# Optimization experiments

Measured on AMD Instinct MI355X. Metric: run time of the kernel, lower is better.

The kernel has to match this reference:

```python
import jax, jax.numpy as jnp
import numpy as np

N, LAT, H, R, L = 384, 64, 128, 16, 3
CUTOFF = 12.0
COORD_INIT_SCALE = 0.001


def setup_inputs() -> dict:
    key = jax.random.key(0)
    ks = jax.random.split(key, 12)
    def w(k, shape, fan):
        return jax.random.normal(k, shape, jnp.float32) / np.float32(np.sqrt(fan))
    return {
        "z": jax.random.normal(ks[0], (N, LAT), jnp.float32),
        # spread anchors so the radius graph is non-trivially sparse
        "anchor_coords": jax.random.normal(ks[1], (N, 3), jnp.float32) * 10.0,
        "proj_W": w(ks[2], (LAT, H), LAT),
        "proj_b": jnp.zeros((H,), jnp.float32),
        "eW1": w(ks[3], (L, 2 * H + R, H), 2 * H + R),
        "eb1": jnp.zeros((L, H), jnp.float32),
        "eW2": w(ks[4], (L, H, H), H),
        "eb2": jnp.zeros((L, H), jnp.float32),
        "nW1": w(ks[5], (L, 2 * H, H), 2 * H),
        "nb1": jnp.zeros((L, H), jnp.float32),
        "nW2": w(ks[6], (L, H, H), H),
        "nb2": jnp.zeros((L, H), jnp.float32),
        "cW1": w(ks[7], (L, H, H), H),
        "cb1": jnp.zeros((L, H), jnp.float32),
        # coord head scaled by coord_update_init_scale for stable coordinate updates
        "cW2": w(ks[8], (L, H, 1), H) * COORD_INIT_SCALE,
    }


def _rbf(d):
    # Gaussian radial basis expansion over [0, cutoff]
    mu = jnp.linspace(0.0, CUTOFF, R, dtype=d.dtype)            # (R,)
    gamma = jnp.asarray((R / CUTOFF) ** 2, d.dtype)
    return jnp.exp(-gamma * (d[..., None] - mu) ** 2)           # (..., R)


def reference(z, anchor_coords, proj_W, proj_b, eW1, eb1, eW2, eb2,
              nW1, nb1, nW2, nb2, cW1, cb1, cW2):
    silu = jax.nn.silu
    n = z.shape[0]
    h = z @ proj_W + proj_b                                      # (N, H)
    x = anchor_coords - anchor_coords.mean(0, keepdims=True)     # (N, 3)

    idx = jnp.arange(n)
    seq_mask = jnp.abs(idx[:, None] - idx[None, :]) == 1         # sequential edges
    eye = jnp.eye(n, dtype=bool)

    for l in range(L):
        # rebuild radius graph from current coords (dense jit-safe mask)
        diff = x[:, None, :] - x[None, :, :]                     # (N, N, 3) x_i - x_j
        d2 = jnp.sum(diff * diff, axis=-1)                       # (N, N)
        mask = ((d2 < CUTOFF ** 2) & ~eye) | seq_mask            # (N, N) bool
        maskf = mask.astype(h.dtype)
        d = jnp.sqrt(jnp.where(mask, d2, 1.0)) * maskf           # NaN-safe sqrt
        e = _rbf(d)                                              # (N, N, R)

        hi = jnp.broadcast_to(h[:, None, :], (n, n, H))          # receiver
        hj = jnp.broadcast_to(h[None, :, :], (n, n, H))          # sender
        m = silu(jnp.concatenate([hi, hj, e], -1) @ eW1[l] + eb1[l])
        m = silu(m @ eW2[l] + eb2[l]) * maskf[..., None]         # (N, N, H) messages

        agg = m.sum(1)                                           # scatter-add at receiver
        h = h + silu(jnp.concatenate([h, agg], -1) @ nW1[l] + nb1[l]) @ nW2[l] + nb2[l]

        w = (silu(m @ cW1[l] + cb1[l]) @ cW2[l]) * maskf[..., None]  # (N, N, 1)
        x = x + jnp.sum(diff * w, axis=1)                        # equivariant coord update
    return x
```

## Files before the change

kernel.cpp:

```cpp
#include <hip/hip_runtime.h>
#include <hip/hip_bf16.h>

#define NN 384
#define CUTOFF2 144.0f
#define GAMMA 1.7777778f

#define PK_L 26624
#define PK_WE 8192
#define PK_W2 10240
#define PK_C1 18432

#define STG_F32 1152
#define EDGE_SMEM ((PK_L + 8*STG_F32)*4)

#define O_XA 0
#define O_XB 4608
#define O_H 9216
#define O_A 205824
#define O_AGG 402432
#define O_HBF 599040
#define O_EREC 697344
#define O_UNITS 3056640
#define O_UCNT 3075072
#define O_PK 3075200

typedef __bf16 bf16x8 __attribute__((ext_vector_type(8)));
typedef float f32x4 __attribute__((ext_vector_type(4)));
typedef unsigned long long u64;

union ER { struct { float dx, dy, dz; unsigned j; } e; uint4 u4; };

__device__ __forceinline__ unsigned short f2bf(float f){
  unsigned u = __float_as_uint(f);
  return (unsigned short)((u + 0x7fffu + ((u >> 16) & 1u)) >> 16);
}
__device__ __forceinline__ unsigned pk2(float a, float b){
  return ((unsigned)f2bf(b) << 16) | f2bf(a);
}
__device__ __forceinline__ float silu(float x){ return x / (1.0f + __expf(-x)); }

__global__ void k_prep(const float* __restrict__ eW1, const float* __restrict__ eW2,
                       const float* __restrict__ cW1, unsigned* __restrict__ pk,
                       const float* __restrict__ anchor, float* __restrict__ xA,
                       float* __restrict__ xB, int* __restrict__ ucnt){
  if (blockIdx.x == 312) {
    __shared__ float ssum[3];
    int t = threadIdx.x;
    if (t < 3) { ssum[t] = 0.f; ucnt[t] = 0; }
    __syncthreads();
    for (int n = t; n < 384; n += 256) {
      atomicAdd(&ssum[0], anchor[n*3]);
      atomicAdd(&ssum[1], anchor[n*3+1]);
      atomicAdd(&ssum[2], anchor[n*3+2]);
    }
    __syncthreads();
    float m0 = ssum[0]*(1.f/384.f), m1 = ssum[1]*(1.f/384.f), m2 = ssum[2]*(1.f/384.f);
    for (int n = t; n < 384; n += 256) {
      float v0 = anchor[n*3]-m0, v1 = anchor[n*3+1]-m1, v2 = anchor[n*3+2]-m2;
      xA[n*3]=v0; xA[n*3+1]=v1; xA[n*3+2]=v2;
      xB[n*3]=v0; xB[n*3+1]=v1; xB[n*3+2]=v2;
    }
    return;
  }
  int t = blockIdx.x * 256 + threadIdx.x;
  int layer = t / PK_L, r = t % PK_L;
  const float* src; int fr; int isWe = 0;
  if (r < PK_WE)        { fr = r;          src = eW1 + (layer*272 + 128)*128; }
  else if (r < PK_W2)   { fr = r - PK_WE;  src = eW1 + (layer*272 + 256)*128; isWe = 1; }
  else if (r < PK_C1)   { fr = r - PK_W2;  src = eW2 + layer*128*128; }
  else                  { fr = r - PK_C1;  src = cW1 + layer*128*128; }
  int tp = fr & 3, l = (fr >> 2) & 63, nc = fr >> 8;
  int n, k;
  if (!isWe) { n = nc >> 2; int c = nc & 3; k = c*32 + ((l>>4)<<3) + 2*tp; }
  else       { n = nc;                      k = ((l>>4)<<3) + 2*tp; }
  int nn = n*16 + (l & 15);
  float w0, w1;
  if (isWe) { w0 = (k < 16)   ? src[k*128+nn]     : 0.f;
              w1 = (k+1 < 16) ? src[(k+1)*128+nn] : 0.f; }
  else      { w0 = src[k*128+nn]; w1 = src[(k+1)*128+nn]; }
  pk[t] = ((unsigned)f2bf(w1) << 16) | f2bf(w0);
}

__device__ __forceinline__ void scan_tail(
    int row, int rowsel, int t256, bool v, const float* __restrict__ x,
    uint4* __restrict__ erec, int* __restrict__ units, int* __restrict__ ucntSlot,
    int* scn){
  int* scnt  = scn + rowsel*2;
  int* sbase = scnt + 1;
  if (t256 == 0) *scnt = 0;
  __syncthreads();
  if (v) {
    float xi0 = x[row*3], xi1 = x[row*3+1], xi2 = x[row*3+2];
    for (int j = t256; j < 384; j += 256) {
      float d0 = xi0-x[j*3], d1 = xi1-x[j*3+1], d2 = xi2-x[j*3+2];
      float dd = d0*d0 + d1*d1 + d2*d2;
      bool msk = ((dd < CUTOFF2) && (j != row)) || (j == row-1) || (j == row+1);
      if (msk) {
        int ss = atomicAdd(scnt, 1);
        ER er; er.e.dx = d0; er.e.dy = d1; er.e.dz = d2; er.e.j = (unsigned)j;
        erec[row*384 + ss] = er.u4;
      }
    }
  }
  __syncthreads();
  if (v) {
    int cnt = *scnt;
    int p = (32 - (cnt & 31)) & 31;
    if (t256 < p) {
      ER er; er.e.dx = 0.f; er.e.dy = 0.f; er.e.dz = 0.f; er.e.j = (unsigned)row;
      erec[row*384 + cnt + t256] = er.u4;
    }
    if (t256 == 0) *sbase = atomicAdd(ucntSlot, (cnt + 31) >> 5);
  }
  __syncthreads();
  if (v) {
    int cnt = *scnt, nu = (cnt + 31) >> 5;
    if (t256 < nu) {
      int nv = cnt - (t256 << 5); if (nv > 32) nv = 32;
      units[*sbase + t256] = row | (t256 << 9) | (nv << 13);
    }
  }
}

__global__ __launch_bounds__(512) void k_projscan(
    const float* __restrict__ z, const float* __restrict__ pW,
    const float* __restrict__ pb, const float* __restrict__ eW1,
    const float* __restrict__ eb1, float* __restrict__ h,
    unsigned short* __restrict__ hbf, float* __restrict__ A,
    float* __restrict__ agg, const float* __restrict__ x,
    uint4* __restrict__ erec, int* __restrict__ units, int* __restrict__ ucntSlot){
  __shared__ float sb2[2*768];
  __shared__ int scn[4];
  const int tid = threadIdx.x;
  const int rowsel = tid >> 8, half = (tid >> 7) & 1, o = tid & 127, t256 = tid & 255;
  const int row = blockIdx.x + 256*rowsel;
  const bool v = row < NN;
  float* sb = sb2 + rowsel*768;
  float* sh = sb; float* part = sb + 512; float* sz = sb + 640;

  if (v) {
    if (half == 0) { if (o < 64) sz[o] = z[row*64 + o]; }
    else           agg[row*128 + o] = 0.f;
  }
  __syncthreads();
  float pp = 0.f;
  if (v) {
    int k0 = half*32;
    float p0=0,p1=0,p2=0,p3=0;
    #pragma unroll 8
    for (int k = k0; k < k0+32; k += 4) {
      p0 += sz[k]   * pW[k*128 + o];
      p1 += sz[k+1] * pW[(k+1)*128 + o];
      p2 += sz[k+2] * pW[(k+2)*128 + o];
      p3 += sz[k+3] * pW[(k+3)*128 + o];
    }
    pp = (p0+p1)+(p2+p3);
    if (half) part[o] = pp;
  }
  __syncthreads();
  if (v && !half) {
    float hh = pb[o] + pp + part[o];
    h[row*128 + o] = hh; sh[o] = hh;
    hbf[row*128 + o] = f2bf(hh);
  }
  __syncthreads();
  float cc = 0.f;
  if (v) {
    int k0 = half*64;
    float c0=0,c1=0,c2=0,c3=0;
    #pragma unroll 16
    for (int k = k0; k < k0+64; k += 4) {
      c0 += sh[k]   * eW1[k*128 + o];
      c1 += sh[k+1] * eW1[(k+1)*128 + o];
      c2 += sh[k+2] * eW1[(k+2)*128 + o];
      c3 += sh[k+3] * eW1[(k+3)*128 + o];
    }
    cc = (c0+c1)+(c2+c3);
    if (half) part[o] = cc;
  }
  __syncthreads();
  if (v && !half) A[row*128 + o] = eb1[o] + cc + part[o];

  scan_tail(row, rowsel, t256, v, x, erec, units, ucntSlot, scn);
}

__global__ __launch_bounds__(512) void k_node(
    const float* __restrict__ nW1, const float* __restrict__ nb1,
    const float* __restrict__ nW2, const float* __restrict__ nb2,
    const float* __restrict__ eW1n, const float* __restrict__ eb1n,
    float* __restrict__ h, unsigned short* __restrict__ hbf,
    float* __restrict__ agg, float* __restrict__ A,
    const float* __restrict__ xsrc, float* __restrict__ xdst,
    uint4* __restrict__ erec, int* __restrict__ units, int* __restrict__ ucntSlot){
  __shared__ float sb2[2*768];
  __shared__ int scn[4];
  const int tid = threadIdx.x;
  const int rowsel = tid >> 8, half = (tid >> 7) & 1, o = tid & 127, t256 = tid & 255;
  const int row = blockIdx.x + 256*rowsel;
  const bool v = row < NN;
  float* sb = sb2 + rowsel*768;
  float* sh = sb; float* sg = sb+128; float* st = sb+256; float* shn = sb+384; float* part = sb+512;

  if (v) {
    if (half == 0) {
      sh[o] = h[row*128 + o];
      if (o < 3) xdst[row*3 + o] = xsrc[row*3 + o];
    } else {
      sg[o] = agg[row*128 + o]; agg[row*128 + o] = 0.f;
    }
  }
  __syncthreads();
  float aa = 0.f;
  if (v) {
    const float* src = half ? sg : sh;
    const float* wb  = nW1 + half*128*128;
    float a0=0,a1=0,a2=0,a3=0;
    #pragma unroll 16
    for (int k = 0; k < 128; k += 4) {
      a0 += src[k]   * wb[k*128 + o];
      a1 += src[k+1] * wb[(k+1)*128 + o];
      a2 += src[k+2] * wb[(k+2)*128 + o];
      a3 += src[k+3] * wb[(k+3)*128 + o];
    }
    aa = (a0+a1)+(a2+a3);
    if (half) part[o] = aa;
  }
  __syncthreads();
  if (v && !half) st[o] = silu(nb1[o] + aa + part[o]);
  __syncthreads();
  float bb = 0.f;
  if (v) {
    int k0 = half*64;
    float b0=0,b1=0,b2=0,b3=0;
    #pragma unroll 16
    for (int k = k0; k < k0+64; k += 4) {
      b0 += st[k]   * nW2[k*128 + o];
      b1 += st[k+1] * nW2[(k+1)*128 + o];
      b2 += st[k+2] * nW2[(k+2)*128 + o];
      b3 += st[k+3] * nW2[(k+3)*128 + o];
    }
    bb = (b0+b1)+(b2+b3);
    if (half) part[o] = bb;
  }
  __syncthreads();
  if (v && !half) {
    float hn = sh[o] + nb2[o] + bb + part[o];
    h[row*128 + o] = hn; shn[o] = hn;
    hbf[row*128 + o] = f2bf(hn);
  }
  __syncthreads();
  float cc = 0.f;
  if (v) {
    int k0 = half*64;
    float c0=0,c1=0,c2=0,c3=0;
    #pragma unroll 16
    for (int k = k0; k < k0+64; k += 4) {
      c0 += shn[k]   * eW1n[k*128 + o];
      c1 += shn[k+1] * eW1n[(k+1)*128 + o];
      c2 += shn[k+2] * eW1n[(k+2)*128 + o];
      c3 += shn[k+3] * eW1n[(k+3)*128 + o];
    }
    cc = (c0+c1)+(c2+c3);
    if (half) part[o] = cc;
  }
  __syncthreads();
  if (v && !half) A[row*128 + o] = eb1n[o] + cc + part[o];

  scan_tail(row, rowsel, t256, v, xsrc, erec, units, ucntSlot, scn);
}

#define TRANSFORM(VA, VB, FA, FB)                                              \
  _Pragma("unroll")                                                            \
  for (int c = 0; c < 4; ++c) {                                                \
    _Pragma("unroll")                                                          \
    for (int tl = 0; tl < 2; ++tl) {                                           \
      int t = 2*c + tl;                                                        \
      _Pragma("unroll")                                                        \
      for (int r = 0; r < 4; ++r) {                                            \
        stg[(quad*4 + r)*36 + tl*16 + col0] = VA[t][r];                        \
        stg[(16 + quad*4 + r)*36 + tl*16 + col0] = VB[t][r];                   \
      }                                                                        \
    }                                                                          \
    float4 lo = *(const float4*)(stg + col0*36 + quad*8);                      \
    float4 hi = *(const float4*)(stg + col0*36 + quad*8 + 4);                  \
    FA[c].u = make_uint4(pk2(lo.x,lo.y), pk2(lo.z,lo.w),                       \
                         pk2(hi.x,hi.y), pk2(hi.z,hi.w));                      \
    float4 lo2 = *(const float4*)(stg + (16 + col0)*36 + quad*8);              \
    float4 hi2 = *(const float4*)(stg + (16 + col0)*36 + quad*8 + 4);          \
    FB[c].u = make_uint4(pk2(lo2.x,lo2.y), pk2(lo2.z,lo2.w),                   \
                         pk2(hi2.x,hi2.y), pk2(hi2.z,hi2.w));                  \
  }

__global__ __launch_bounds__(512, 1) void k_edge(
    float* __restrict__ x_out, const float* __restrict__ Ag,
    const unsigned short* __restrict__ hbf, const uint4* __restrict__ erec,
    const int* __restrict__ units, const int* __restrict__ Ucnt,
    float* __restrict__ agg, const unsigned* __restrict__ pkl,
    const float* __restrict__ eb2g, const float* __restrict__ cb1g,
    const float* __restrict__ cw2g){
  extern __shared__ unsigned smem[];
  const int tid = threadIdx.x, q = tid & 63, s = tid >> 6;
  const int U = Ucnt[0];
  if (blockIdx.x >= U) return;

  for (int idx = tid; idx < PK_L/4; idx += 512)
    ((uint4*)smem)[idx] = ((const uint4*)pkl)[idx];
  __syncthreads();

  const int col0 = q & 15, quad = q >> 4;
  float eb2v[8], cb1v[8], cw2v[8];
  #pragma unroll
  for (int t = 0; t < 8; ++t) {
    int c = t*16 + col0;
    eb2v[t] = eb2g[c]; cb1v[t] = cb1g[c]; cw2v[t] = cw2g[c];
  }
  float* stg = (float*)(smem + PK_L) + s*STG_F32;
  const f32x4 z4 = {0.f, 0.f, 0.f, 0.f};
  union U8 { uint4 u; bf16x8 v; };

  for (int u = blockIdx.x + 256*s; u < U; u += 2048) {
    const int desc = units[u];
    const int i = desc & 511, b = (desc >> 9) & 15, nvalid = (desc >> 13) & 63;
    float Aval[8];
    #pragma unroll
    for (int t = 0; t < 8; ++t) Aval[t] = Ag[i*128 + t*16 + col0];
    ER e0, e1;
    e0.u4 = erec[i*384 + b*32 + col0];
    e1.u4 = erec[i*384 + b*32 + 16 + col0];
    const int j0 = (int)e0.e.j, j1 = (int)e1.e.j;
    const float d0x = e0.e.dx, d0y = e0.e.dy, d0z = e0.e.dz;
    const float d1x = e1.e.dx, d1y = e1.e.dy, d1z = e1.e.dz;
    const float dd0 = sqrtf(d0x*d0x + d0y*d0y + d0z*d0z);
    const float dd1 = sqrtf(d1x*d1x + d1y*d1y + d1z*d1z);

    U8 ha0[4], ha1[4];
    #pragma unroll
    for (int c = 0; c < 4; ++c) {
      ha0[c].u = *(const uint4*)(hbf + j0*128 + c*32 + quad*8);
      ha1[c].u = *(const uint4*)(hbf + j1*128 + c*32 + quad*8);
    }

    U8 cve0, cve1;
    if (q < 32) {
      #pragma unroll
      for (int tp = 0; tp < 4; ++tp) {
        float k0 = (float)(quad*8 + 2*tp);
        float t00 = dd0 - 0.8f*k0, t01 = dd0 - 0.8f*(k0+1.f);
        float t10 = dd1 - 0.8f*k0, t11 = dd1 - 0.8f*(k0+1.f);
        (&cve0.u.x)[tp] = pk2(__expf(-GAMMA*t00*t00), __expf(-GAMMA*t01*t01));
        (&cve1.u.x)[tp] = pk2(__expf(-GAMMA*t10*t10), __expf(-GAMMA*t11*t11));
      }
    } else { cve0.u = make_uint4(0,0,0,0); cve1.u = make_uint4(0,0,0,0); }

    f32x4 acc0[8], acc1[8];
    #pragma unroll
    for (int t = 0; t < 8; ++t) { acc0[t] = z4; acc1[t] = z4; }
    #pragma unroll
    for (int t = 0; t < 8; ++t) {
      #pragma unroll
      for (int c = 0; c < 4; ++c) {
        bf16x8 w = *(const bf16x8*)(smem + ((t*4 + c)*64 + q)*4);
        acc0[t] = __builtin_amdgcn_mfma_f32_16x16x32_bf16(ha0[c].v, w, acc0[t], 0, 0, 0);
        acc1[t] = __builtin_amdgcn_mfma_f32_16x16x32_bf16(ha1[c].v, w, acc1[t], 0, 0, 0);
      }
      bf16x8 we = *(const bf16x8*)(smem + PK_WE + (t*64 + q)*4);
      acc0[t] = __builtin_amdgcn_mfma_f32_16x16x32_bf16(cve0.v, we, acc0[t], 0, 0, 0);
      acc1[t] = __builtin_amdgcn_mfma_f32_16x16x32_bf16(cve1.v, we, acc1[t], 0, 0, 0);
    }
    #pragma unroll
    for (int t = 0; t < 8; ++t)
      #pragma unroll
      for (int r = 0; r < 4; ++r) {
        acc0[t][r] = silu(acc0[t][r] + Aval[t]);
        acc1[t][r] = silu(acc1[t][r] + Aval[t]);
      }

    U8 a20[4], a21[4];
    TRANSFORM(acc0, acc1, a20, a21);

    f32x4 m0[8], m1v[8];
    #pragma unroll
    for (int t = 0; t < 8; ++t) { m0[t] = z4; m1v[t] = z4; }
    #pragma unroll
    for (int t = 0; t < 8; ++t)
      #pragma unroll
      for (int c = 0; c < 4; ++c) {
        bf16x8 w = *(const bf16x8*)(smem + PK_W2 + ((t*4 + c)*64 + q)*4);
        m0[t] = __builtin_amdgcn_mfma_f32_16x16x32_bf16(a20[c].v, w, m0[t], 0, 0, 0);
        m1v[t] = __builtin_amdgcn_mfma_f32_16x16x32_bf16(a21[c].v, w, m1v[t], 0, 0, 0);
      }
    #pragma unroll
    for (int t = 0; t < 8; ++t) {
      float cs = 0.f;
      #pragma unroll
      for (int r = 0; r < 4; ++r) {
        m0[t][r] = silu(m0[t][r] + eb2v[t]);
        m1v[t][r] = silu(m1v[t][r] + eb2v[t]);
        if (quad*4 + r < nvalid) cs += m0[t][r];
        if (16 + quad*4 + r < nvalid) cs += m1v[t][r];
      }
      cs += __shfl_xor(cs, 16); cs += __shfl_xor(cs, 32);
      if (q < 16) atomicAdd(&agg[i*128 + t*16 + q], cs);
    }

    U8 a30[4], a31[4];
    TRANSFORM(m0, m1v, a30, a31);

    f32x4 c30[8], c31[8];
    #pragma unroll
    for (int t = 0; t < 8; ++t) { c30[t] = z4; c31[t] = z4; }
    #pragma unroll
    for (int t = 0; t < 8; ++t)
      #pragma unroll
      for (int c = 0; c < 4; ++c) {
        bf16x8 w = *(const bf16x8*)(smem + PK_C1 + ((t*4 + c)*64 + q)*4);
        c30[t] = __builtin_amdgcn_mfma_f32_16x16x32_bf16(a30[c].v, w, c30[t], 0, 0, 0);
        c31[t] = __builtin_amdgcn_mfma_f32_16x16x32_bf16(a31[c].v, w, c31[t], 0, 0, 0);
      }
    float p0[4], p1[4];
    #pragma unroll
    for (int r = 0; r < 4; ++r) {
      float pa = 0.f, pb = 0.f;
      #pragma unroll
      for (int t = 0; t < 8; ++t) {
        pa += silu(c30[t][r] + cb1v[t]) * cw2v[t];
        pb += silu(c31[t][r] + cb1v[t]) * cw2v[t];
      }
      if (quad*4 + r >= nvalid) pa = 0.f;
      if (16 + quad*4 + r >= nvalid) pb = 0.f;
      p0[r] = pa; p1[r] = pb;
    }
    #pragma unroll
    for (int r = 0; r < 4; ++r)
      #pragma unroll
      for (int off = 1; off < 16; off <<= 1) {
        p0[r] += __shfl_xor(p0[r], off);
        p1[r] += __shfl_xor(p1[r], off);
      }
    float dx0 = 0.f, dx1 = 0.f, dx2 = 0.f;
    #pragma unroll
    for (int r = 0; r < 4; ++r) {
      int el = quad*4 + r;
      float s0 = __shfl(d0x, el), s1 = __shfl(d0y, el), s2 = __shfl(d0z, el);
      if (col0 == 0) { dx0 += p0[r]*s0; dx1 += p0[r]*s1; dx2 += p0[r]*s2; }
      float u0 = __shfl(d1x, el), u1 = __shfl(d1y, el), u2 = __shfl(d1z, el);
      if (col0 == 0) { dx0 += p1[r]*u0; dx1 += p1[r]*u1; dx2 += p1[r]*u2; }
    }
    dx0 += __shfl_xor(dx0, 16); dx0 += __shfl_xor(dx0, 32);
    dx1 += __shfl_xor(dx1, 16); dx1 += __shfl_xor(dx1, 32);
    dx2 += __shfl_xor(dx2, 16); dx2 += __shfl_xor(dx2, 32);
    if (q == 0) {
      atomicAdd(&x_out[i*3 + 0], dx0);
      atomicAdd(&x_out[i*3 + 1], dx1);
      atomicAdd(&x_out[i*3 + 2], dx2);
    }
  }
}

extern "C" void kernel_launch(void* const* d_in, const int* in_sizes, int n_in,
                              void* d_out, int out_size, void* d_ws, size_t ws_size,
                              hipStream_t stream){
  const float* z      = (const float*)d_in[0];
  const float* anchor = (const float*)d_in[1];
  const float* projW  = (const float*)d_in[2];
  const float* projb  = (const float*)d_in[3];
  const float* eW1    = (const float*)d_in[4];
  const float* eb1    = (const float*)d_in[5];
  const float* eW2    = (const float*)d_in[6];
  const float* eb2    = (const float*)d_in[7];
  const float* nW1    = (const float*)d_in[8];
  const float* nb1    = (const float*)d_in[9];
  const float* nW2    = (const float*)d_in[10];
  const float* nb2    = (const float*)d_in[11];
  const float* cW1    = (const float*)d_in[12];
  const float* cb1    = (const float*)d_in[13];
  const float* cW2    = (const float*)d_in[14];
  float* out = (float*)d_out;

  char* w = (char*)d_ws;
  float* xA  = (float*)(w + O_XA);
  float* xB  = (float*)(w + O_XB);
  float* h   = (float*)(w + O_H);
  float* A   = (float*)(w + O_A);
  float* agg = (float*)(w + O_AGG);
  unsigned short* hbf = (unsigned short*)(w + O_HBF);
  uint4* erec = (uint4*)(w + O_EREC);
  int* units = (int*)(w + O_UNITS);
  int* ucnt  = (int*)(w + O_UCNT);
  unsigned* pk = (unsigned*)(w + O_PK);

  hipFuncSetAttribute((const void*)k_edge, hipFuncAttributeMaxDynamicSharedMemorySize, EDGE_SMEM);

  k_prep<<<313, 256, 0, stream>>>(eW1, eW2, cW1, pk, anchor, xA, xB, ucnt);
  k_projscan<<<256, 512, 0, stream>>>(z, projW, projb, eW1, eb1, h, hbf, A, agg,
                                      xA, erec, units, ucnt + 0);
  k_edge<<<256, 512, EDGE_SMEM, stream>>>(xB, A, hbf, erec, units, ucnt + 0,
                                          agg, pk, eb2, cb1, cW2);
  k_node<<<256, 512, 0, stream>>>(nW1, nb1, nW2, nb2, eW1 + 272*128, eb1 + 128,
                                  h, hbf, agg, A, xB, xA, erec, units, ucnt + 1);
  k_edge<<<256, 512, EDGE_SMEM, stream>>>(xA, A, hbf, erec, units, ucnt + 1,
                                          agg, pk + PK_L, eb2 + 128, cb1 + 128, cW2 + 128);
  k_node<<<256, 512, 0, stream>>>(nW1 + 256*128, nb1 + 128, nW2 + 128*128, nb2 + 128,
                                  eW1 + 2*272*128, eb1 + 256,
                                  h, hbf, agg, A, xA, out, erec, units, ucnt + 2);
  k_edge<<<256, 512, EDGE_SMEM, stream>>>(out, A, hbf, erec, units, ucnt + 2,
                                          agg, pk + 2*PK_L, eb2 + 256, cb1 + 256, cW2 + 256);
}
```

Before: 191.1 us.

## Merge prep and projection kernels, defer centering, stage node weights in LDS

Measured after the change: 196.1 us. 2.6% more time.

```diff
diff --git a/kernel.cpp b/kernel.cpp
--- a/kernel.cpp
+++ b/kernel.cpp
@@ -22,11 +22,11 @@
 #define O_EREC 697344
 #define O_UNITS 3056640
 #define O_UCNT 3075072
+#define O_MEAN 3075136
 #define O_PK 3075200
 
 typedef __bf16 bf16x8 __attribute__((ext_vector_type(8)));
 typedef float f32x4 __attribute__((ext_vector_type(4)));
-typedef unsigned long long u64;
 
 union ER { struct { float dx, dy, dz; unsigned j; } e; uint4 u4; };
 
@@ -39,30 +39,10 @@
 }
 __device__ __forceinline__ float silu(float x){ return x / (1.0f + __expf(-x)); }
 
-__global__ void k_prep(const float* __restrict__ eW1, const float* __restrict__ eW2,
-                       const float* __restrict__ cW1, unsigned* __restrict__ pk,
-                       const float* __restrict__ anchor, float* __restrict__ xA,
-                       float* __restrict__ xB, int* __restrict__ ucnt){
-  if (blockIdx.x == 312) {
-    __shared__ float ssum[3];
-    int t = threadIdx.x;
-    if (t < 3) { ssum[t] = 0.f; ucnt[t] = 0; }
-    __syncthreads();
-    for (int n = t; n < 384; n += 256) {
-      atomicAdd(&ssum[0], anchor[n*3]);
-      atomicAdd(&ssum[1], anchor[n*3+1]);
-      atomicAdd(&ssum[2], anchor[n*3+2]);
-    }
-    __syncthreads();
-    float m0 = ssum[0]*(1.f/384.f), m1 = ssum[1]*(1.f/384.f), m2 = ssum[2]*(1.f/384.f);
-    for (int n = t; n < 384; n += 256) {
-      float v0 = anchor[n*3]-m0, v1 = anchor[n*3+1]-m1, v2 = anchor[n*3+2]-m2;
-      xA[n*3]=v0; xA[n*3+1]=v1; xA[n*3+2]=v2;
-      xB[n*3]=v0; xB[n*3+1]=v1; xB[n*3+2]=v2;
-    }
-    return;
-  }
-  int t = blockIdx.x * 256 + threadIdx.x;
+__device__ __forceinline__ void pack_one(int t, const float* __restrict__ eW1,
+                                         const float* __restrict__ eW2,
+                                         const float* __restrict__ cW1,
+                                         unsigned* __restrict__ pk){
   int layer = t / PK_L, r = t % PK_L;
   const float* src; int fr; int isWe = 0;
   if (r < PK_WE)        { fr = r;          src = eW1 + (layer*272 + 128)*128; }
@@ -81,17 +61,17 @@
   pk[t] = ((unsigned)f2bf(w1) << 16) | f2bf(w0);
 }
 
-__device__ __forceinline__ void scan_tail(
-    int row, int rowsel, int t256, bool v, const float* __restrict__ x,
+__device__ __forceinline__ void scan3(
+    int row, int rsel, int o, bool v, const float* __restrict__ x,
     uint4* __restrict__ erec, int* __restrict__ units, int* __restrict__ ucntSlot,
     int* scn){
-  int* scnt  = scn + rowsel*2;
+  int* scnt  = scn + rsel*2;
   int* sbase = scnt + 1;
-  if (t256 == 0) *scnt = 0;
+  if (v && o == 0) *scnt = 0;
   __syncthreads();
   if (v) {
     float xi0 = x[row*3], xi1 = x[row*3+1], xi2 = x[row*3+2];
-    for (int j = t256; j < 384; j += 256) {
+    for (int j = o; j < 384; j += 128) {
       float d0 = xi0-x[j*3], d1 = xi1-x[j*3+1], d2 = xi2-x[j*3+2];
       float dd = d0*d0 + d1*d1 + d2*d2;
       bool msk = ((dd < CUTOFF2) && (j != row)) || (j == row-1) || (j == row+1);
@@ -106,167 +86,180 @@
   if (v) {
     int cnt = *scnt;
     int p = (32 - (cnt & 31)) & 31;
-    if (t256 < p) {
+    if (o < p) {
       ER er; er.e.dx = 0.f; er.e.dy = 0.f; er.e.dz = 0.f; er.e.j = (unsigned)row;
-      erec[row*384 + cnt + t256] = er.u4;
-    }
-    if (t256 == 0) *sbase = atomicAdd(ucntSlot, (cnt + 31) >> 5);
+      erec[row*384 + cnt + o] = er.u4;
+    }
+    if (o == 0) *sbase = atomicAdd(ucntSlot, (cnt + 31) >> 5);
   }
   __syncthreads();
   if (v) {
     int cnt = *scnt, nu = (cnt + 31) >> 5;
-    if (t256 < nu) {
-      int nv = cnt - (t256 << 5); if (nv > 32) nv = 32;
-      units[*sbase + t256] = row | (t256 << 9) | (nv << 13);
-    }
-  }
-}
-
-__global__ __launch_bounds__(512) void k_projscan(
-    const float* __restrict__ z, const float* __restrict__ pW,
-    const float* __restrict__ pb, const float* __restrict__ eW1,
+    if (o < nu) {
+      int nv = cnt - (o << 5); if (nv > 32) nv = 32;
+      units[*sbase + o] = row | (o << 9) | (nv << 13);
+    }
+  }
+}
+
+__global__ __launch_bounds__(512) void k_init(
+    const float* __restrict__ eW1, const float* __restrict__ eW2,
+    const float* __restrict__ cW1, unsigned* __restrict__ pk,
+    const float* __restrict__ anchor, const float* __restrict__ z,
+    const float* __restrict__ pW, const float* __restrict__ pbias,
     const float* __restrict__ eb1, float* __restrict__ h,
     unsigned short* __restrict__ hbf, float* __restrict__ A,
-    float* __restrict__ agg, const float* __restrict__ x,
-    uint4* __restrict__ erec, int* __restrict__ units, int* __restrict__ ucntSlot){
-  __shared__ float sb2[2*768];
-  __shared__ int scn[4];
-  const int tid = threadIdx.x;
-  const int rowsel = tid >> 8, half = (tid >> 7) & 1, o = tid & 127, t256 = tid & 255;
-  const int row = blockIdx.x + 256*rowsel;
-  const bool v = row < NN;
-  float* sb = sb2 + rowsel*768;
-  float* sh = sb; float* part = sb + 512; float* sz = sb + 640;
-
-  if (v) {
-    if (half == 0) { if (o < 64) sz[o] = z[row*64 + o]; }
-    else           agg[row*128 + o] = 0.f;
-  }
-  __syncthreads();
-  float pp = 0.f;
-  if (v) {
-    int k0 = half*32;
-    float p0=0,p1=0,p2=0,p3=0;
-    #pragma unroll 8
-    for (int k = k0; k < k0+32; k += 4) {
-      p0 += sz[k]   * pW[k*128 + o];
-      p1 += sz[k+1] * pW[(k+1)*128 + o];
-      p2 += sz[k+2] * pW[(k+2)*128 + o];
-      p3 += sz[k+3] * pW[(k+3)*128 + o];
-    }
-    pp = (p0+p1)+(p2+p3);
-    if (half) part[o] = pp;
-  }
-  __syncthreads();
-  if (v && !half) {
-    float hh = pb[o] + pp + part[o];
-    h[row*128 + o] = hh; sh[o] = hh;
-    hbf[row*128 + o] = f2bf(hh);
-  }
-  __syncthreads();
-  float cc = 0.f;
-  if (v) {
-    int k0 = half*64;
-    float c0=0,c1=0,c2=0,c3=0;
+    float* __restrict__ agg, float* __restrict__ xB, float* __restrict__ meanw,
+    uint4* __restrict__ erec, int* __restrict__ units, int* __restrict__ ucnt0){
+  const int b = blockIdx.x, tid = threadIdx.x;
+  if (b < 156) { pack_one(b*512 + tid, eW1, eW2, cW1, pk); return; }
+  if (b == 156) {
+    __shared__ float ssum[3];
+    if (tid < 3) ssum[tid] = 0.f;
+    __syncthreads();
+    if (tid < 384) {
+      atomicAdd(&ssum[0], anchor[tid*3]);
+      atomicAdd(&ssum[1], anchor[tid*3+1]);
+      atomicAdd(&ssum[2], anchor[tid*3+2]);
+    }
+    __syncthreads();
+    if (tid < 3) meanw[tid] = ssum[tid]*(1.f/384.f);
+    return;
+  }
+  __shared__ float wt[8192];
+  __shared__ float sh[3][128];
+  __shared__ float sz[3][64];
+  __shared__ int scn[6];
+  const int o = tid & 127, rsel = tid >> 7;
+  const int row = (b - 157)*3 + rsel;
+  const bool v = rsel < 3;
+  if (v) {
+    if (o < 64) sz[rsel][o] = z[row*64 + o];
+    agg[row*128 + o] = 0.f;
+    if (o < 3) xB[row*3 + o] = anchor[row*3 + o];
+  }
+  {
+    const float4* g = (const float4*)pW;
+    #pragma unroll
+    for (int i = 0; i < 4; ++i) ((float4*)wt)[tid + 512*i] = g[tid + 512*i];
+  }
+  __syncthreads();
+  float a0=0,a1=0,a2=0,a3=0;
+  if (v) {
     #pragma unroll 16
-    for (int k = k0; k < k0+64; k += 4) {
-      c0 += sh[k]   * eW1[k*128 + o];
-      c1 += sh[k+1] * eW1[(k+1)*128 + o];
-      c2 += sh[k+2] * eW1[(k+2)*128 + o];
-      c3 += sh[k+3] * eW1[(k+3)*128 + o];
-    }
-    cc = (c0+c1)+(c2+c3);
-    if (half) part[o] = cc;
-  }
-  __syncthreads();
-  if (v && !half) A[row*128 + o] = eb1[o] + cc + part[o];
-
-  scan_tail(row, rowsel, t256, v, x, erec, units, ucntSlot, scn);
+    for (int kk = 0; kk < 64; kk += 4) {
+      a0 += sz[rsel][kk]  *wt[kk*128+o];     a1 += sz[rsel][kk+1]*wt[(kk+1)*128+o];
+      a2 += sz[rsel][kk+2]*wt[(kk+2)*128+o]; a3 += sz[rsel][kk+3]*wt[(kk+3)*128+o];
+    }
+  }
+  __syncthreads();
+  if (v) {
+    float hh = pbias[o] + (a0+a1)+(a2+a3);
+    sh[rsel][o] = hh; h[row*128 + o] = hh; hbf[row*128 + o] = f2bf(hh);
+  }
+  __syncthreads();
+  a0=a1=a2=a3=0;
+  for (int t = 0; t < 2; ++t) {
+    const float4* g = (const float4*)(eW1 + t*8192);
+    #pragma unroll
+    for (int i = 0; i < 4; ++i) ((float4*)wt)[tid + 512*i] = g[tid + 512*i];
+    __syncthreads();
+    if (v) {
+      const float* s = &sh[rsel][t*64];
+      #pragma unroll 16
+      for (int kk = 0; kk < 64; kk += 4) {
+        a0 += s[kk]  *wt[kk*128+o];     a1 += s[kk+1]*wt[(kk+1)*128+o];
+        a2 += s[kk+2]*wt[(kk+2)*128+o]; a3 += s[kk+3]*wt[(kk+3)*128+o];
+      }
+    }
+    __syncthreads();
+  }
+  if (v) A[row*128 + o] = eb1[o] + (a0+a1)+(a2+a3);
+  scan3(row, rsel, o, v, anchor, erec, units, ucnt0, scn);
 }
 
 __global__ __launch_bounds__(512) void k_node(
-    const float* __restrict__ nW1, const float* __restrict__ nb1,
-    const float* __restrict__ nW2, const float* __restrict__ nb2,
-    const float* __restrict__ eW1n, const float* __restrict__ eb1n,
+    const float* __restrict__ nW1l, const float* __restrict__ nb1l,
+    const float* __restrict__ nW2l, const float* __restrict__ nb2l,
+    const float* __restrict__ eW1a, const float* __restrict__ eb1a,
     float* __restrict__ h, unsigned short* __restrict__ hbf,
     float* __restrict__ agg, float* __restrict__ A,
     const float* __restrict__ xsrc, float* __restrict__ xdst,
+    const float* __restrict__ meanp,
     uint4* __restrict__ erec, int* __restrict__ units, int* __restrict__ ucntSlot){
-  __shared__ float sb2[2*768];
-  __shared__ int scn[4];
-  const int tid = threadIdx.x;
-  const int rowsel = tid >> 8, half = (tid >> 7) & 1, o = tid & 127, t256 = tid & 255;
-  const int row = blockIdx.x + 256*rowsel;
-  const bool v = row < NN;
-  float* sb = sb2 + rowsel*768;
-  float* sh = sb; float* sg = sb+128; float* st = sb+256; float* shn = sb+384; float* part = sb+512;
-
-  if (v) {
-    if (half == 0) {
-      sh[o] = h[row*128 + o];
-      if (o < 3) xdst[row*3 + o] = xsrc[row*3 + o];
-    } else {
-      sg[o] = agg[row*128 + o]; agg[row*128 + o] = 0.f;
-    }
-  }
-  __syncthreads();
-  float aa = 0.f;
-  if (v) {
-    const float* src = half ? sg : sh;
-    const float* wb  = nW1 + half*128*128;
-    float a0=0,a1=0,a2=0,a3=0;
-    #pragma unroll 16
-    for (int k = 0; k < 128; k += 4) {
-      a0 += src[k]   * wb[k*128 + o];
-      a1 += src[k+1] * wb[(k+1)*128 + o];
-      a2 += src[k+2] * wb[(k+2)*128 + o];
-      a3 += src[k+3] * wb[(k+3)*128 + o];
-    }
-    aa = (a0+a1)+(a2+a3);
-    if (half) part[o] = aa;
-  }
-  __syncthreads();
-  if (v && !half) st[o] = silu(nb1[o] + aa + part[o]);
-  __syncthreads();
-  float bb = 0.f;
-  if (v) {
-    int k0 = half*64;
-    float b0=0,b1=0,b2=0,b3=0;
-    #pragma unroll 16
-    for (int k = k0; k < k0+64; k += 4) {
-      b0 += st[k]   * nW2[k*128 + o];
-      b1 += st[k+1] * nW2[(k+1)*128 + o];
-      b2 += st[k+2] * nW2[(k+2)*128 + o];
-      b3 += st[k+3] * nW2[(k+3)*128 + o];
-    }
-    bb = (b0+b1)+(b2+b3);
-    if (half) part[o] = bb;
-  }
-  __syncthreads();
-  if (v && !half) {
-    float hn = sh[o] + nb2[o] + bb + part[o];
-    h[row*128 + o] = hn; shn[o] = hn;
-    hbf[row*128 + o] = f2bf(hn);
-  }
-  __syncthreads();
-  float cc = 0.f;
-  if (v) {
-    int k0 = half*64;
-    float c0=0,c1=0,c2=0,c3=0;
-    #pragma unroll 16
-    for (int k = k0; k < k0+64; k += 4) {
-      c0 += shn[k]   * eW1n[k*128 + o];
-      c1 += shn[k+1] * eW1n[(k+1)*128 + o];
-      c2 += shn[k+2] * eW1n[(k+2)*128 + o];
-      c3 += shn[k+3] * eW1n[(k+3)*128 + o];
-    }
-    cc = (c0+c1)+(c2+c3);
-    if (half) part[o] = cc;
-  }
-  __syncthreads();
-  if (v && !half) A[row*128 + o] = eb1n[o] + cc + part[o];
-
-  scan_tail(row, rowsel, t256, v, xsrc, erec, units, ucntSlot, scn);
+  __shared__ float wt[8192];
+  __shared__ float sh[3][128], sg[3][128], st[3][128], shn[3][128];
+  __shared__ int scn[6];
+  const int tid = threadIdx.x, o = tid & 127, rsel = tid >> 7;
+  const int row = blockIdx.x*3 + rsel;
+  const bool v = rsel < 3;
+  if (v) {
+    sh[rsel][o] = h[row*128 + o];
+    sg[rsel][o] = agg[row*128 + o];
+    agg[row*128 + o] = 0.f;
+    if (o < 3) {
+      float m = meanp ? meanp[o] : 0.f;
+      xdst[row*3 + o] = xsrc[row*3 + o] - m;
+    }
+  }
+  __syncthreads();
+  float a0=0,a1=0,a2=0,a3=0;
+  for (int t = 0; t < 4; ++t) {
+    const float4* g = (const float4*)(nW1l + t*8192);
+    #pragma unroll
+    for (int i = 0; i < 4; ++i) ((float4*)wt)[tid + 512*i] = g[tid + 512*i];
+    __syncthreads();
+    if (v) {
+      const float* s = (t < 2) ? &sh[rsel][t*64] : &sg[rsel][(t-2)*64];
+      #pragma unroll 16
+      for (int kk = 0; kk < 64; kk += 4) {
+        a0 += s[kk]  *wt[kk*128+o];     a1 += s[kk+1]*wt[(kk+1)*128+o];
+        a2 += s[kk+2]*wt[(kk+2)*128+o]; a3 += s[kk+3]*wt[(kk+3)*128+o];
+      }
+    }
+    __syncthreads();
+  }
+  if (v) st[rsel][o] = silu(nb1l[o] + (a0+a1)+(a2+a3));
+  __syncthreads();
+  a0=a1=a2=a3=0;
+  for (int t = 0; t < 2; ++t) {
+    const float4* g = (const float4*)(nW2l + t*8192);
+    #pragma unroll
+    for (int i = 0; i < 4; ++i) ((float4*)wt)[tid + 512*i] = g[tid + 512*i];
+    __syncthreads();
+    if (v) {
+      const float* s = &st[rsel][t*64];
+      #pragma unroll 16
+      for (int kk = 0; kk < 64; kk += 4) {
+        a0 += s[kk]  *wt[kk*128+o];     a1 += s[kk+1]*wt[(kk+1)*128+o];
+        a2 += s[kk+2]*wt[(kk+2)*128+o]; a3 += s[kk+3]*wt[(kk+3)*128+o];
+      }
+    }
+    __syncthreads();
+  }
+  if (v) {
+    float hn = sh[rsel][o] + nb2l[o] + (a0+a1)+(a2+a3);
+    h[row*128 + o] = hn; hbf[row*128 + o] = f2bf(hn); shn[rsel][o] = hn;
+  }
+  __syncthreads();
+  a0=a1=a2=a3=0;
+  for (int t = 0; t < 2; ++t) {
+    const float4* g = (const float4*)(eW1a + t*8192);
+    #pragma unroll
+    for (int i = 0; i < 4; ++i) ((float4*)wt)[tid + 512*i] = g[tid + 512*i];
+    __syncthreads();
+    if (v) {
+      const float* s = &shn[rsel][t*64];
+      #pragma unroll 16
+      for (int kk = 0; kk < 64; kk += 4) {
+        a0 += s[kk]  *wt[kk*128+o];     a1 += s[kk+1]*wt[(kk+1)*128+o];
+        a2 += s[kk+2]*wt[(kk+2)*128+o]; a3 += s[kk+3]*wt[(kk+3)*128+o];
+      }
+    }
+    __syncthreads();
+  }
+  if (v) A[row*128 + o] = eb1a[o] + (a0+a1)+(a2+a3);
+  scan3(row, rsel, o, v, xsrc, erec, units, ucntSlot, scn);
 }
 
 #define TRANSFORM(VA, VB, FA, FB)                                              \
@@ -487,22 +480,25 @@
   uint4* erec = (uint4*)(w + O_EREC);
   int* units = (int*)(w + O_UNITS);
   int* ucnt  = (int*)(w + O_UCNT);
+  float* meanw = (float*)(w + O_MEAN);
   unsigned* pk = (unsigned*)(w + O_PK);
 
   hipFuncSetAttribute((const void*)k_edge, hipFuncAttributeMaxDynamicSharedMemorySize, EDGE_SMEM);
 
-  k_prep<<<313, 256, 0, stream>>>(eW1, eW2, cW1, pk, anchor, xA, xB, ucnt);
-  k_projscan<<<256, 512, 0, stream>>>(z, projW, projb, eW1, eb1, h, hbf, A, agg,
-                                      xA, erec, units, ucnt + 0);
+  hipMemsetAsync(ucnt, 0, 12, stream);
+  k_init<<<285, 512, 0, stream>>>(eW1, eW2, cW1, pk, anchor, z, projW, projb,
+                                  eb1, h, hbf, A, agg, xB, meanw, erec, units, ucnt + 0);
   k_edge<<<256, 512, EDGE_SMEM, stream>>>(xB, A, hbf, erec, units, ucnt + 0,
                                           agg, pk, eb2, cb1, cW2);
-  k_node<<<256, 512, 0, stream>>>(nW1, nb1, nW2, nb2, eW1 + 272*128, eb1 + 128,
-                                  h, hbf, agg, A, xB, xA, erec, units, ucnt + 1);
+  k_node<<<128, 512, 0, stream>>>(nW1, nb1, nW2, nb2, eW1 + 272*128, eb1 + 128,
+                                  h, hbf, agg, A, xB, xA, (const float*)nullptr,
+                                  erec, units, ucnt + 1);
   k_edge<<<256, 512, EDGE_SMEM, stream>>>(xA, A, hbf, erec, units, ucnt + 1,
                                           agg, pk + PK_L, eb2 + 128, cb1 + 128, cW2 + 128);
-  k_node<<<256, 512, 0, stream>>>(nW1 + 256*128, nb1 + 128, nW2 + 128*128, nb2 + 128,
+  k_node<<<128, 512, 0, stream>>>(nW1 + 256*128, nb1 + 128, nW2 + 128*128, nb2 + 128,
                                   eW1 + 2*272*128, eb1 + 256,
-                                  h, hbf, agg, A, xA, out, erec, units, ucnt + 2);
+                                  h, hbf, agg, A, xA, out, meanw,
+                                  erec, units, ucnt + 2);
   k_edge<<<256, 512, EDGE_SMEM, stream>>>(out, A, hbf, erec, units, ucnt + 2,
                                           agg, pk + 2*PK_L, eb2 + 256, cb1 + 256, cW2 + 256);
 }
```

## Fuse weight packing, projection and first radius scan; defer coordinate centering

Applied to the files above, without the earlier changes.

After: 189.1 us. Within noise of the previous version (-1.1%).

```diff
diff --git a/kernel.cpp b/kernel.cpp
--- a/kernel.cpp
+++ b/kernel.cpp
@@ -22,11 +22,11 @@
 #define O_EREC 697344
 #define O_UNITS 3056640
 #define O_UCNT 3075072
+#define O_MEAN 3075136
 #define O_PK 3075200
 
 typedef __bf16 bf16x8 __attribute__((ext_vector_type(8)));
 typedef float f32x4 __attribute__((ext_vector_type(4)));
-typedef unsigned long long u64;
 
 union ER { struct { float dx, dy, dz; unsigned j; } e; uint4 u4; };
 
@@ -38,48 +38,6 @@
   return ((unsigned)f2bf(b) << 16) | f2bf(a);
 }
 __device__ __forceinline__ float silu(float x){ return x / (1.0f + __expf(-x)); }
-
-__global__ void k_prep(const float* __restrict__ eW1, const float* __restrict__ eW2,
-                       const float* __restrict__ cW1, unsigned* __restrict__ pk,
-                       const float* __restrict__ anchor, float* __restrict__ xA,
-                       float* __restrict__ xB, int* __restrict__ ucnt){
-  if (blockIdx.x == 312) {
-    __shared__ float ssum[3];
-    int t = threadIdx.x;
-    if (t < 3) { ssum[t] = 0.f; ucnt[t] = 0; }
-    __syncthreads();
-    for (int n = t; n < 384; n += 256) {
-      atomicAdd(&ssum[0], anchor[n*3]);
-      atomicAdd(&ssum[1], anchor[n*3+1]);
-      atomicAdd(&ssum[2], anchor[n*3+2]);
-    }
-    __syncthreads();
-    float m0 = ssum[0]*(1.f/384.f), m1 = ssum[1]*(1.f/384.f), m2 = ssum[2]*(1.f/384.f);
-    for (int n = t; n < 384; n += 256) {
-      float v0 = anchor[n*3]-m0, v1 = anchor[n*3+1]-m1, v2 = anchor[n*3+2]-m2;
-      xA[n*3]=v0; xA[n*3+1]=v1; xA[n*3+2]=v2;
-      xB[n*3]=v0; xB[n*3+1]=v1; xB[n*3+2]=v2;
-    }
-    return;
-  }
-  int t = blockIdx.x * 256 + threadIdx.x;
-  int layer = t / PK_L, r = t % PK_L;
-  const float* src; int fr; int isWe = 0;
-  if (r < PK_WE)        { fr = r;          src = eW1 + (layer*272 + 128)*128; }
-  else if (r < PK_W2)   { fr = r - PK_WE;  src = eW1 + (layer*272 + 256)*128; isWe = 1; }
-  else if (r < PK_C1)   { fr = r - PK_W2;  src = eW2 + layer*128*128; }
-  else                  { fr = r - PK_C1;  src = cW1 + layer*128*128; }
-  int tp = fr & 3, l = (fr >> 2) & 63, nc = fr >> 8;
-  int n, k;
-  if (!isWe) { n = nc >> 2; int c = nc & 3; k = c*32 + ((l>>4)<<3) + 2*tp; }
-  else       { n = nc;                      k = ((l>>4)<<3) + 2*tp; }
-  int nn = n*16 + (l & 15);
-  float w0, w1;
-  if (isWe) { w0 = (k < 16)   ? src[k*128+nn]     : 0.f;
-              w1 = (k+1 < 16) ? src[(k+1)*128+nn] : 0.f; }
-  else      { w0 = src[k*128+nn]; w1 = src[(k+1)*128+nn]; }
-  pk[t] = ((unsigned)f2bf(w1) << 16) | f2bf(w0);
-}
 
 __device__ __forceinline__ void scan_tail(
     int row, int rowsel, int t256, bool v, const float* __restrict__ x,
@@ -122,29 +80,62 @@
   }
 }
 
-__global__ __launch_bounds__(512) void k_projscan(
-    const float* __restrict__ z, const float* __restrict__ pW,
-    const float* __restrict__ pb, const float* __restrict__ eW1,
+__global__ __launch_bounds__(512) void k_init(
+    const float* __restrict__ eW1, const float* __restrict__ eW2,
+    const float* __restrict__ cW1, unsigned* __restrict__ pk,
+    const float* __restrict__ anchor, const float* __restrict__ z,
+    const float* __restrict__ pW, const float* __restrict__ pb,
     const float* __restrict__ eb1, float* __restrict__ h,
     unsigned short* __restrict__ hbf, float* __restrict__ A,
-    float* __restrict__ agg, const float* __restrict__ x,
-    uint4* __restrict__ erec, int* __restrict__ units, int* __restrict__ ucntSlot){
+    float* __restrict__ agg, float* __restrict__ xB, float* __restrict__ meanw,
+    uint4* __restrict__ erec, int* __restrict__ units, int* __restrict__ ucnt0){
+  const int b = blockIdx.x, tid = threadIdx.x;
+  if (b < 156) {
+    int t = b*512 + tid;
+    int layer = t / PK_L, r = t % PK_L;
+    const float* src; int fr; int isWe = 0;
+    if (r < PK_WE)        { fr = r;          src = eW1 + (layer*272 + 128)*128; }
+    else if (r < PK_W2)   { fr = r - PK_WE;  src = eW1 + (layer*272 + 256)*128; isWe = 1; }
+    else if (r < PK_C1)   { fr = r - PK_W2;  src = eW2 + layer*128*128; }
+    else                  { fr = r - PK_C1;  src = cW1 + layer*128*128; }
+    int tp = fr & 3, l = (fr >> 2) & 63, nc = fr >> 8;
+    int n, k;
+    if (!isWe) { n = nc >> 2; int c = nc & 3; k = c*32 + ((l>>4)<<3) + 2*tp; }
+    else       { n = nc;                      k = ((l>>4)<<3) + 2*tp; }
+    int nn = n*16 + (l & 15);
+    float w0, w1;
+    if (isWe) { w0 = (k < 16)   ? src[k*128+nn]     : 0.f;
+                w1 = (k+1 < 16) ? src[(k+1)*128+nn] : 0.f; }
+    else      { w0 = src[k*128+nn]; w1 = src[(k+1)*128+nn]; }
+    pk[t] = ((unsigned)f2bf(w1) << 16) | f2bf(w0);
+    return;
+  }
+  if (b == 156) {
+    __shared__ float ssum[3];
+    if (tid < 3) ssum[tid] = 0.f;
+    __syncthreads();
+    if (tid < 384) {
+      atomicAdd(&ssum[0], anchor[tid*3]);
+      atomicAdd(&ssum[1], anchor[tid*3+1]);
+      atomicAdd(&ssum[2], anchor[tid*3+2]);
+    }
+    __syncthreads();
+    if (tid < 3) meanw[tid] = ssum[tid]*(1.f/384.f);
+    return;
+  }
   __shared__ float sb2[2*768];
   __shared__ int scn[4];
-  const int tid = threadIdx.x;
   const int rowsel = tid >> 8, half = (tid >> 7) & 1, o = tid & 127, t256 = tid & 255;
-  const int row = blockIdx.x + 256*rowsel;
-  const bool v = row < NN;
+  const int row = (b - 157)*2 + rowsel;
   float* sb = sb2 + rowsel*768;
   float* sh = sb; float* part = sb + 512; float* sz = sb + 640;
 
-  if (v) {
-    if (half == 0) { if (o < 64) sz[o] = z[row*64 + o]; }
-    else           agg[row*128 + o] = 0.f;
-  }
+  if (half == 0) { if (o < 64) sz[o] = z[row*64 + o]; }
+  else           agg[row*128 + o] = 0.f;
+  if (half == 0 && o < 3) xB[row*3 + o] = anchor[row*3 + o];
   __syncthreads();
   float pp = 0.f;
-  if (v) {
+  {
     int k0 = half*32;
     float p0=0,p1=0,p2=0,p3=0;
     #pragma unroll 8
@@ -158,14 +149,14 @@
     if (half) part[o] = pp;
   }
   __syncthreads();
-  if (v && !half) {
+  if (!half) {
     float hh = pb[o] + pp + part[o];
     h[row*128 + o] = hh; sh[o] = hh;
     hbf[row*128 + o] = f2bf(hh);
   }
   __syncthreads();
   float cc = 0.f;
-  if (v) {
+  {
     int k0 = half*64;
     float c0=0,c1=0,c2=0,c3=0;
     #pragma unroll 16
@@ -179,9 +170,9 @@
     if (half) part[o] = cc;
   }
   __syncthreads();
-  if (v && !half) A[row*128 + o] = eb1[o] + cc + part[o];
-
-  scan_tail(row, rowsel, t256, v, x, erec, units, ucntSlot, scn);
+  if (!half) A[row*128 + o] = eb1[o] + cc + part[o];
+
+  scan_tail(row, rowsel, t256, true, anchor, erec, units, ucnt0, scn);
 }
 
 __global__ __launch_bounds__(512) void k_node(
@@ -191,6 +182,7 @@
     float* __restrict__ h, unsigned short* __restrict__ hbf,
     float* __restrict__ agg, float* __restrict__ A,
     const float* __restrict__ xsrc, float* __restrict__ xdst,
+    const float* __restrict__ meanp,
     uint4* __restrict__ erec, int* __restrict__ units, int* __restrict__ ucntSlot){
   __shared__ float sb2[2*768];
   __shared__ int scn[4];
@@ -204,7 +196,10 @@
   if (v) {
     if (half == 0) {
       sh[o] = h[row*128 + o];
-      if (o < 3) xdst[row*3 + o] = xsrc[row*3 + o];
+      if (o < 3) {
+        float m = meanp ? meanp[o] : 0.f;
+        xdst[row*3 + o] = xsrc[row*3 + o] - m;
+      }
     } else {
       sg[o] = agg[row*128 + o]; agg[row*128 + o] = 0.f;
     }
@@ -487,22 +482,25 @@
   uint4* erec = (uint4*)(w + O_EREC);
   int* units = (int*)(w + O_UNITS);
   int* ucnt  = (int*)(w + O_UCNT);
+  float* meanw = (float*)(w + O_MEAN);
   unsigned* pk = (unsigned*)(w + O_PK);
 
   hipFuncSetAttribute((const void*)k_edge, hipFuncAttributeMaxDynamicSharedMemorySize, EDGE_SMEM);
 
-  k_prep<<<313, 256, 0, stream>>>(eW1, eW2, cW1, pk, anchor, xA, xB, ucnt);
-  k_projscan<<<256, 512, 0, stream>>>(z, projW, projb, eW1, eb1, h, hbf, A, agg,
-                                      xA, erec, units, ucnt + 0);
+  hipMemsetAsync(ucnt, 0, 12, stream);
+  k_init<<<349, 512, 0, stream>>>(eW1, eW2, cW1, pk, anchor, z, projW, projb,
+                                  eb1, h, hbf, A, agg, xB, meanw, erec, units, ucnt + 0);
   k_edge<<<256, 512, EDGE_SMEM, stream>>>(xB, A, hbf, erec, units, ucnt + 0,
                                           agg, pk, eb2, cb1, cW2);
   k_node<<<256, 512, 0, stream>>>(nW1, nb1, nW2, nb2, eW1 + 272*128, eb1 + 128,
-                                  h, hbf, agg, A, xB, xA, erec, units, ucnt + 1);
+                                  h, hbf, agg, A, xB, xA, (const float*)nullptr,
+                                  erec, units, ucnt + 1);
   k_edge<<<256, 512, EDGE_SMEM, stream>>>(xA, A, hbf, erec, units, ucnt + 1,
                                           agg, pk + PK_L, eb2 + 128, cb1 + 128, cW2 + 128);
   k_node<<<256, 512, 0, stream>>>(nW1 + 256*128, nb1 + 128, nW2 + 128*128, nb2 + 128,
                                   eW1 + 2*272*128, eb1 + 256,
-                                  h, hbf, agg, A, xA, out, erec, units, ucnt + 2);
+                                  h, hbf, agg, A, xA, out, meanw,
+                                  erec, units, ucnt + 2);
   k_edge<<<256, 512, EDGE_SMEM, stream>>>(out, A, hbf, erec, units, ucnt + 2,
                                           agg, pk + 2*PK_L, eb2 + 256, cb1 + 256, cW2 + 256);
 }
```
